# Kernel optimization log

Hardware: AMD Instinct MI355X
Metric: run time of the kernel (lower is better)

The kernel has to match this reference:

```python
import jax, jax.numpy as jnp
import numpy as np
from jax.scipy.special import erf

# Module constants from init_kwargs
SIGMA = 1.0
NORM_FACTOR = 90.0474
TWOPI = 2.0 * np.pi
N_ATOMS = 4096


def setup_inputs() -> dict:
    key = jax.random.key(0)
    k1, k2 = jax.random.split(key)
    q = jax.random.normal(k1, (N_ATOMS,), dtype=jnp.float32)
    # positions in a ~40 Angstrom box
    r = jax.random.uniform(k2, (N_ATOMS, 3), dtype=jnp.float32) * 40.0
    # singular cell (det < 1e-6) selects the real-space branch, as in the torch code
    cell = jnp.zeros((1, 3, 3), dtype=jnp.float32)
    batch = jnp.zeros((N_ATOMS,), dtype=jnp.int32)  # single system
    return {"q": q, "r": r, "cell": cell, "batch": batch}


def _realspace_pot(q, r):
    # q: [n], r: [n,3] -> scalar potential (n_q = 1)
    norm_const = NORM_FACTOR / TWOPI
    a = 1.0 / (SIGMA * np.sqrt(2.0))
    n = r.shape[0]
    off = ~jnp.eye(n, dtype=bool)                       # mask self-interaction
    r_ij = r[None, :, :] - r[:, None, :]                # [n,n,3]
    d2 = jnp.sum(r_ij * r_ij, axis=-1)                  # [n,n]
    dist = jnp.sqrt(jnp.where(off, d2, 1.0))            # safe sqrt on diagonal
    rinv = jnp.where(off, 1.0 / dist, 0.0)
    erf_t = jnp.where(off, erf(dist * a), 0.0)
    f_qq = erf_t * rinv * norm_const                    # [n,n]
    # 0.5 * sum_ij q_i f_qq_ij q_j  (remove_self_interaction=True -> no self term)
    return 0.5 * jnp.einsum('i,ij,j->', q, f_qq, q)


def reference(q, r, cell, batch):
    # batch is all-zeros (single system); zero cell -> real-space branch.
    # torch forward: stack per-batch pots [1, n_q=1], sum over dim=1 -> shape [1]
    pot = _realspace_pot(q, r)
    return pot[None]
```

## Files before the change

kernel.cpp:

```cpp
#include <hip/hip_runtime.h>
#include <math.h>


#define N_ATOMS 4096
#define T       64
#define K       (N_ATOMS / T)
#define NBLOCKS (K * (K + 1) / 2)

__device__ __forceinline__ float erf_fast(float x) {
    const float p  = 0.3275911f;
    const float a1 = 0.254829592f, a2 = -0.284496736f, a3 = 1.421413741f,
                a4 = -1.453152027f, a5 = 1.061405429f;
    float t = __builtin_amdgcn_rcpf(fmaf(p, x, 1.0f));
    float poly = fmaf(fmaf(fmaf(fmaf(a5, t, a4), t, a3), t, a2), t, a1) * t;
    float e = __builtin_amdgcn_exp2f(-x * x * 1.4426950408889634f);
    return fmaf(-poly, e, 1.0f);
}

__global__ __launch_bounds__(T) void ewald_tri_kernel(
    const float* __restrict__ q,
    const float* __restrict__ r,
    float* __restrict__ partial)
{
    __shared__ float4 s4[T];

    const int t = blockIdx.x;
    int row = (int)((sqrtf(fmaf(8.0f, (float)t, 1.0f)) - 1.0f) * 0.5f);
    while ((row + 1) * (row + 2) / 2 <= t) ++row;
    while (row * (row + 1) / 2 > t) --row;
    const int ib = row;
    const int jb = t - row * (row + 1) / 2;

    const int lane = threadIdx.x;
    const int i    = ib * T + lane;
    const int j0   = jb * T;

    {
        const int j = j0 + lane;
        s4[lane] = make_float4(r[3 * j + 0], r[3 * j + 1], r[3 * j + 2], q[j]);
    }
    __syncthreads();

    const float xi = r[3 * i + 0];
    const float yi = r[3 * i + 1];
    const float zi = r[3 * i + 2];
    const float qi = q[i];
    const float a  = 0.70710678118654752f;

    float acc = 0.0f;
    if (ib == jb) {
        #pragma unroll 8
        for (int jj = 0; jj < T; ++jj) {
            const float4 v = s4[jj];
            const float dx = xi - v.x, dy = yi - v.y, dz = zi - v.z;
            float d2 = fmaf(dx, dx, fmaf(dy, dy, dz * dz));
            const float m = (jj != lane) ? 1.0f : 0.0f;
            d2 += 1.0f - m;
            const float dinv = __builtin_amdgcn_rsqf(d2);
            const float dist = d2 * dinv;
            const float f = erf_fast(dist * a) * dinv;
            acc = fmaf(m * v.w, f, acc);
        }
    } else {
        #pragma unroll 8
        for (int jj = 0; jj < T; ++jj) {
            const float4 v = s4[jj];
            const float dx = xi - v.x, dy = yi - v.y, dz = zi - v.z;
            const float d2 = fmaf(dx, dx, fmaf(dy, dy, dz * dz));
            const float dinv = __builtin_amdgcn_rsqf(d2);
            float f = dinv;
            if (__any(d2 < 31.0f)) {
                const float dist = d2 * dinv;
                f = erf_fast(dist * a) * dinv;
            }
            acc = fmaf(v.w, f, acc);
        }
        acc *= 2.0f;
    }
    acc *= qi;

    for (int off = 32; off > 0; off >>= 1)
        acc += __shfl_down(acc, off, 64);
    if (lane == 0) partial[blockIdx.x] = acc;
}

__global__ __launch_bounds__(256) void ewald_reduce_kernel(
    const float* __restrict__ partial,
    float* __restrict__ out)
{
    const int tid = threadIdx.x;
    float v = 0.0f;
    #pragma unroll
    for (int k = 0; k < (NBLOCKS + 255) / 256; ++k) {
        const int idx = tid + k * 256;
        if (idx < NBLOCKS) v += partial[idx];
    }

    for (int off = 32; off > 0; off >>= 1)
        v += __shfl_down(v, off, 64);

    __shared__ float wsum[256 / 64];
    if ((tid & 63) == 0) wsum[tid >> 6] = v;
    __syncthreads();
    if (tid == 0) {
        float s = 0.0f;
        #pragma unroll
        for (int w = 0; w < 256 / 64; ++w) s += wsum[w];
        const float norm_const = 90.0474f / (2.0f * 3.14159265358979f);
        out[0] = 0.5f * s * norm_const;
    }
}

extern "C" void kernel_launch(void* const* d_in, const int* in_sizes, int n_in,
                              void* d_out, int out_size, void* d_ws, size_t ws_size,
                              hipStream_t stream) {
    const float* q = (const float*)d_in[0];
    const float* r = (const float*)d_in[1];
    float* out     = (float*)d_out;
    float* partial = (float*)d_ws;

    ewald_tri_kernel<<<NBLOCKS, T, 0, stream>>>(q, r, partial);
    ewald_reduce_kernel<<<1, 256, 0, stream>>>(partial, out);
}
```

Measured before the change: 17.09 us.

## Fuse reduction into main kernel via last-block atomic counter, pack four tiles per block

Each block now handles four triangular 64x64 tiles, one per wavefront, instead of one tile per 64-thread block. The separate reduce kernel is replaced by a last-block-done pattern: every block stores its partial sum and bumps an atomic counter, and the final block sums all partials and writes the output. This removes one kernel launch but adds a memset launch, an atomic, and a fence per block. The partials buffer (520 floats) fits below the 4096-byte offset used for the counter.

```diff
diff --git a/kernel.cpp b/kernel.cpp
--- a/kernel.cpp
+++ b/kernel.cpp
@@ -5,7 +5,10 @@
 #define N_ATOMS 4096
 #define T       64
 #define K       (N_ATOMS / T)
-#define NBLOCKS (K * (K + 1) / 2)
+#define NTILES  (K * (K + 1) / 2)
+#define WPB     4
+#define BLOCK   (WPB * 64)
+#define NBLOCKS (NTILES / WPB)
 
 __device__ __forceinline__ float erf_fast(float x) {
     const float p  = 0.3275911f;
@@ -17,29 +20,35 @@
     return fmaf(-poly, e, 1.0f);
 }
 
-__global__ __launch_bounds__(T) void ewald_tri_kernel(
+__global__ __launch_bounds__(BLOCK) void ewald_fused_kernel(
     const float* __restrict__ q,
     const float* __restrict__ r,
-    float* __restrict__ partial)
+    float* __restrict__ partial,
+    unsigned int* __restrict__ cnt,
+    float* __restrict__ out)
 {
-    __shared__ float4 s4[T];
+    __shared__ float4 s4[WPB][T];
+    __shared__ float  wacc[WPB];
+    __shared__ int    isLast;
 
-    const int t = blockIdx.x;
-    int row = (int)((sqrtf(fmaf(8.0f, (float)t, 1.0f)) - 1.0f) * 0.5f);
-    while ((row + 1) * (row + 2) / 2 <= t) ++row;
-    while (row * (row + 1) / 2 > t) --row;
+    const int tid  = threadIdx.x;
+    const int wid  = tid >> 6;
+    const int lane = tid & 63;
+    const int tt   = blockIdx.x * WPB + wid;
+
+    int row = (int)((sqrtf(fmaf(8.0f, (float)tt, 1.0f)) - 1.0f) * 0.5f);
+    while ((row + 1) * (row + 2) / 2 <= tt) ++row;
+    while (row * (row + 1) / 2 > tt) --row;
     const int ib = row;
-    const int jb = t - row * (row + 1) / 2;
+    const int jb = tt - row * (row + 1) / 2;
 
-    const int lane = threadIdx.x;
-    const int i    = ib * T + lane;
-    const int j0   = jb * T;
+    const int i  = ib * T + lane;
+    const int j0 = jb * T;
 
     {
         const int j = j0 + lane;
-        s4[lane] = make_float4(r[3 * j + 0], r[3 * j + 1], r[3 * j + 2], q[j]);
+        s4[wid][lane] = make_float4(r[3 * j + 0], r[3 * j + 1], r[3 * j + 2], q[j]);
     }
-    __syncthreads();
 
     const float xi = r[3 * i + 0];
     const float yi = r[3 * i + 1];
@@ -51,20 +60,19 @@
     if (ib == jb) {
         #pragma unroll 8
         for (int jj = 0; jj < T; ++jj) {
-            const float4 v = s4[jj];
+            const float4 v = s4[wid][jj];
             const float dx = xi - v.x, dy = yi - v.y, dz = zi - v.z;
             float d2 = fmaf(dx, dx, fmaf(dy, dy, dz * dz));
             const float m = (jj != lane) ? 1.0f : 0.0f;
             d2 += 1.0f - m;
             const float dinv = __builtin_amdgcn_rsqf(d2);
             const float dist = d2 * dinv;
-            const float f = erf_fast(dist * a) * dinv;
-            acc = fmaf(m * v.w, f, acc);
+            acc = fmaf(m * v.w, erf_fast(dist * a) * dinv, acc);
         }
     } else {
         #pragma unroll 8
         for (int jj = 0; jj < T; ++jj) {
-            const float4 v = s4[jj];
+            const float4 v = s4[wid][jj];
             const float dx = xi - v.x, dy = yi - v.y, dz = zi - v.z;
             const float d2 = fmaf(dx, dx, fmaf(dy, dy, dz * dz));
             const float dinv = __builtin_amdgcn_rsqf(d2);
@@ -81,33 +89,34 @@
 
     for (int off = 32; off > 0; off >>= 1)
         acc += __shfl_down(acc, off, 64);
-    if (lane == 0) partial[blockIdx.x] = acc;
-}
+    if (lane == 0) wacc[wid] = acc;
+    __syncthreads();
 
-__global__ __launch_bounds__(256) void ewald_reduce_kernel(
-    const float* __restrict__ partial,
-    float* __restrict__ out)
-{
-    const int tid = threadIdx.x;
-    float v = 0.0f;
-    #pragma unroll
-    for (int k = 0; k < (NBLOCKS + 255) / 256; ++k) {
-        const int idx = tid + k * 256;
-        if (idx < NBLOCKS) v += partial[idx];
+    if (tid == 0) {
+        const float s = wacc[0] + wacc[1] + wacc[2] + wacc[3];
+        __hip_atomic_store(&partial[blockIdx.x], s,
+                           __ATOMIC_RELAXED, __HIP_MEMORY_SCOPE_AGENT);
+        __threadfence();
+        const unsigned int old = __hip_atomic_fetch_add(
+            cnt, 1u, __ATOMIC_ACQ_REL, __HIP_MEMORY_SCOPE_AGENT);
+        isLast = (old == NBLOCKS - 1);
     }
+    __syncthreads();
 
-    for (int off = 32; off > 0; off >>= 1)
-        v += __shfl_down(v, off, 64);
-
-    __shared__ float wsum[256 / 64];
-    if ((tid & 63) == 0) wsum[tid >> 6] = v;
-    __syncthreads();
-    if (tid == 0) {
-        float s = 0.0f;
-        #pragma unroll
-        for (int w = 0; w < 256 / 64; ++w) s += wsum[w];
-        const float norm_const = 90.0474f / (2.0f * 3.14159265358979f);
-        out[0] = 0.5f * s * norm_const;
+    if (isLast) {
+        float v = 0.0f;
+        for (int idx = tid; idx < NBLOCKS; idx += BLOCK)
+            v += __hip_atomic_load(&partial[idx],
+                                   __ATOMIC_RELAXED, __HIP_MEMORY_SCOPE_AGENT);
+        for (int off = 32; off > 0; off >>= 1)
+            v += __shfl_down(v, off, 64);
+        if (lane == 0) wacc[wid] = v;
+        __syncthreads();
+        if (tid == 0) {
+            const float s = wacc[0] + wacc[1] + wacc[2] + wacc[3];
+            const float norm_const = 90.0474f / (2.0f * 3.14159265358979f);
+            out[0] = 0.5f * s * norm_const;
+        }
     }
 }
 
@@ -118,7 +127,8 @@
     const float* r = (const float*)d_in[1];
     float* out     = (float*)d_out;
     float* partial = (float*)d_ws;
+    unsigned int* cnt = (unsigned int*)((char*)d_ws + 4096);
 
-    ewald_tri_kernel<<<NBLOCKS, T, 0, stream>>>(q, r, partial);
-    ewald_reduce_kernel<<<1, 256, 0, stream>>>(partial, out);
+    hipMemsetAsync(cnt, 0, sizeof(unsigned int), stream);
+    ewald_fused_kernel<<<NBLOCKS, BLOCK, 0, stream>>>(q, r, partial, cnt, out);
 }
```

New measurement: 32.11 us. 1.88x slower.

## Split pair tiles into 64x16 per-wave chunks with four waves per block

Applied to the files above, without the earlier changes.

Replaces the 64x64 triangular block tiling with per-wave tiles of 64 rows by 16 columns, packed four waves per 256-thread block. The aim is four times as many waves, each with a shorter loop, to improve occupancy and latency hiding. Diagonal tiles now mask with j < i, so only the strict lower triangle is summed; this drops the factor of two and the final 0.5. The wave-uniform skip of the erf term for far pairs is removed, so every pair evaluates erf. Staging into shared memory now relies on ordering within a single wave instead of a block barrier.

```diff
diff --git a/kernel.cpp b/kernel.cpp
--- a/kernel.cpp
+++ b/kernel.cpp
@@ -3,9 +3,11 @@
 
 
 #define N_ATOMS 4096
-#define T       64
-#define K       (N_ATOMS / T)
-#define NBLOCKS (K * (K + 1) / 2)
+#define JC      16
+#define WPB     4
+#define BLOCK   (WPB * 64)
+#define NWAVES  8320
+#define NBLOCKS (NWAVES / WPB)
 
 __device__ __forceinline__ float erf_fast(float x) {
     const float p  = 0.3275911f;
@@ -17,29 +19,31 @@
     return fmaf(-poly, e, 1.0f);
 }
 
-__global__ __launch_bounds__(T) void ewald_tri_kernel(
+__global__ __launch_bounds__(BLOCK) void ewald_pair_kernel(
     const float* __restrict__ q,
     const float* __restrict__ r,
     float* __restrict__ partial)
 {
-    __shared__ float4 s4[T];
+    __shared__ float4 s4[WPB][JC];
+    __shared__ float  wacc[WPB];
 
-    const int t = blockIdx.x;
-    int row = (int)((sqrtf(fmaf(8.0f, (float)t, 1.0f)) - 1.0f) * 0.5f);
-    while ((row + 1) * (row + 2) / 2 <= t) ++row;
-    while (row * (row + 1) / 2 > t) --row;
-    const int ib = row;
-    const int jb = t - row * (row + 1) / 2;
+    const int tid  = threadIdx.x;
+    const int wid  = tid >> 6;
+    const int lane = tid & 63;
+    const int tt   = blockIdx.x * WPB + wid;
 
-    const int lane = threadIdx.x;
-    const int i    = ib * T + lane;
-    const int j0   = jb * T;
+    int ib = (int)((sqrtf(fmaf(2.0f, (float)tt, 1.0f)) - 1.0f) * 0.5f);
+    while (2 * (ib + 1) * (ib + 2) <= tt) ++ib;
+    while (2 * ib * (ib + 1) > tt) --ib;
+    const int jt = tt - 2 * ib * (ib + 1);
 
-    {
+    const int i  = ib * 64 + lane;
+    const int j0 = jt * JC;
+
+    if (lane < JC) {
         const int j = j0 + lane;
-        s4[lane] = make_float4(r[3 * j + 0], r[3 * j + 1], r[3 * j + 2], q[j]);
+        s4[wid][lane] = make_float4(r[3 * j + 0], r[3 * j + 1], r[3 * j + 2], q[j]);
     }
-    __syncthreads();
 
     const float xi = r[3 * i + 0];
     const float yi = r[3 * i + 1];
@@ -48,40 +52,39 @@
     const float a  = 0.70710678118654752f;
 
     float acc = 0.0f;
-    if (ib == jb) {
-        #pragma unroll 8
-        for (int jj = 0; jj < T; ++jj) {
-            const float4 v = s4[jj];
-            const float dx = xi - v.x, dy = yi - v.y, dz = zi - v.z;
-            float d2 = fmaf(dx, dx, fmaf(dy, dy, dz * dz));
-            const float m = (jj != lane) ? 1.0f : 0.0f;
-            d2 += 1.0f - m;
-            const float dinv = __builtin_amdgcn_rsqf(d2);
-            const float dist = d2 * dinv;
-            const float f = erf_fast(dist * a) * dinv;
-            acc = fmaf(m * v.w, f, acc);
-        }
-    } else {
-        #pragma unroll 8
-        for (int jj = 0; jj < T; ++jj) {
-            const float4 v = s4[jj];
+    if ((jt >> 2) < ib) {
+        #pragma unroll
+        for (int jj = 0; jj < JC; ++jj) {
+            const float4 v = s4[wid][jj];
             const float dx = xi - v.x, dy = yi - v.y, dz = zi - v.z;
             const float d2 = fmaf(dx, dx, fmaf(dy, dy, dz * dz));
             const float dinv = __builtin_amdgcn_rsqf(d2);
-            float f = dinv;
-            if (__any(d2 < 31.0f)) {
-                const float dist = d2 * dinv;
-                f = erf_fast(dist * a) * dinv;
-            }
-            acc = fmaf(v.w, f, acc);
+            const float x = d2 * dinv * a;
+            acc = fmaf(v.w, erf_fast(x) * dinv, acc);
         }
-        acc *= 2.0f;
+    } else {
+        #pragma unroll
+        for (int jj = 0; jj < JC; ++jj) {
+            const float4 v = s4[wid][jj];
+            const int   jg = j0 + jj;
+            const float dx = xi - v.x, dy = yi - v.y, dz = zi - v.z;
+            float d2 = fmaf(dx, dx, fmaf(dy, dy, dz * dz));
+            const bool ok = (jg < i);
+            const float qj = ok ? v.w : 0.0f;
+            d2 = ok ? d2 : 1.0f;
+            const float dinv = __builtin_amdgcn_rsqf(d2);
+            const float x = d2 * dinv * a;
+            acc = fmaf(qj, erf_fast(x) * dinv, acc);
+        }
     }
     acc *= qi;
 
     for (int off = 32; off > 0; off >>= 1)
         acc += __shfl_down(acc, off, 64);
-    if (lane == 0) partial[blockIdx.x] = acc;
+    if (lane == 0) wacc[wid] = acc;
+    __syncthreads();
+    if (tid == 0)
+        partial[blockIdx.x] = wacc[0] + wacc[1] + wacc[2] + wacc[3];
 }
 
 __global__ __launch_bounds__(256) void ewald_reduce_kernel(
@@ -107,7 +110,7 @@
         #pragma unroll
         for (int w = 0; w < 256 / 64; ++w) s += wsum[w];
         const float norm_const = 90.0474f / (2.0f * 3.14159265358979f);
-        out[0] = 0.5f * s * norm_const;
+        out[0] = s * norm_const;
     }
 }
 
@@ -119,6 +122,6 @@
     float* out     = (float*)d_out;
     float* partial = (float*)d_ws;
 
-    ewald_tri_kernel<<<NBLOCKS, T, 0, stream>>>(q, r, partial);
+    ewald_pair_kernel<<<NBLOCKS, BLOCK, 0, stream>>>(q, r, partial);
     ewald_reduce_kernel<<<1, 256, 0, stream>>>(partial, out);
 }
```

Result: faster. 14.76 us (-13.7%).
